# Kernel optimization log

Hardware: AMD Instinct MI355X
Metric: run time of the kernel (lower is better)

Reference implementation:

```python
import jax, jax.numpy as jnp
import numpy as np

B = 1024          # batch
H = 1024          # rnn_num_hidden
T = 512           # max_length (encoder timesteps)
NUM = 44          # numeric features
EMB = [(30490, 64), (7, 8), (12, 8), (3, 4)]
IN = NUM + sum(d for _, d in EMB)   # input_size = 128


def lstm_cell(x, h, c, w_ih, w_hh, b_ih, b_hh):
    # PyTorch LSTM gate order: i, f, g, o
    g = x @ w_ih.T + h @ w_hh.T + b_ih + b_hh
    i, f, gg, o = jnp.split(g, 4, axis=-1)
    c2 = jax.nn.sigmoid(f) * c + jax.nn.sigmoid(i) * jnp.tanh(gg)
    h2 = jax.nn.sigmoid(o) * jnp.tanh(c2)
    return h2, c2


def setup_inputs():
    key = jax.random.key(0)
    ks = iter(jax.random.split(key, 32))
    nrm = lambda shape, s=0.02: (s * jax.random.normal(next(ks), shape)).astype(jnp.float32)
    return {
        "x": nrm((B, 1, NUM), 1.0),
        "x_emb": jax.random.randint(next(ks), (B, 1, 4), 0, 3),
        "h0": nrm((2, B, H), 1.0),
        "c0": nrm((2, B, H), 1.0),
        "encoder_outputs": nrm((T, B, H), 1.0),
        "emb0": nrm(EMB[0]), "emb1": nrm(EMB[1]), "emb2": nrm(EMB[2]), "emb3": nrm(EMB[3]),
        "attn_w": nrm((T, IN + 2 * H)), "attn_b": nrm((T,)),
        "comb_w": nrm((IN, IN + H)), "comb_b": nrm((IN,)),
        "w_ih0": nrm((4 * H, IN)), "w_hh0": nrm((4 * H, H)),
        "b_ih0": nrm((4 * H,)), "b_hh0": nrm((4 * H,)),
        "w_ih1": nrm((4 * H, H)), "w_hh1": nrm((4 * H, H)),
        "b_ih1": nrm((4 * H,)), "b_hh1": nrm((4 * H,)),
        "pred_w": nrm((1, H)), "pred_b": nrm((1,)),
    }


def reference(x, x_emb, h0, c0, encoder_outputs, emb0, emb1, emb2, emb3,
              attn_w, attn_b, comb_w, comb_b,
              w_ih0, w_hh0, b_ih0, b_hh0, w_ih1, w_hh1, b_ih1, b_hh1,
              pred_w, pred_b):
    xt = x.transpose(1, 0, 2)[0]                       # (B, NUM)
    ids = x_emb.transpose(1, 0, 2)[0]                  # (B, 4)
    e = jnp.concatenate([emb0[ids[:, 0]], emb1[ids[:, 1]],
                         emb2[ids[:, 2]], emb3[ids[:, 3]]], axis=1)
    x_rnn = jnp.concatenate([xt, e], axis=1)           # (B, IN)
    attn_in = jnp.concatenate([x_rnn, h0[0], c0[0]], axis=1)       # (B, IN+2H)
    aw = jax.nn.softmax(attn_in @ attn_w.T + attn_b, axis=1)       # (B, T)
    ctx = jnp.einsum('bt,tbh->bh', aw, encoder_outputs)            # (B, H)
    comb = jnp.concatenate([x_rnn, ctx], axis=1) @ comb_w.T + comb_b  # (B, IN)
    h1, c1 = lstm_cell(comb, h0[0], c0[0], w_ih0, w_hh0, b_ih0, b_hh0)
    h2, c2 = lstm_cell(h1, h0[1], c0[1], w_ih1, w_hh1, b_ih1, b_hh1)
    out = h2 @ pred_w.T + pred_b                       # (B, 1)
    return out, (jnp.stack([h1, h2]), jnp.stack([c1, c2])), aw
```

## Files before the change

kernel.cpp:

```cpp
#include <hip/hip_runtime.h>
#include <hip/hip_bf16.h>

#define B 1024
#define H 1024
#define T 512
#define NUM 44
#define IN 128
#define AK (IN + 2 * H)
#define XC (IN + H)
#define G4 (4 * H)

typedef __attribute__((ext_vector_type(8))) short s16x8;
typedef __attribute__((ext_vector_type(4))) float f32x4;

__device__ __forceinline__ unsigned short f2bf(float f) {
    unsigned u = __float_as_uint(f);
    unsigned r = (u + 0x7fffu + ((u >> 16) & 1u)) >> 16;
    return (unsigned short)r;
}

__device__ __forceinline__ void gload16(const ushort* g, ushort* l) {
    __builtin_amdgcn_global_load_lds(
        (const __attribute__((address_space(1))) void*)g,
        (__attribute__((address_space(3))) void*)l,
        16, 0, 0);
}

#define TM 128
#define TN 128
#define TK 32

__device__ __forceinline__ void gemm_core(
    const ushort* __restrict__ X, const ushort* __restrict__ W,
    const float* __restrict__ bias1, const float* __restrict__ bias2,
    const float* __restrict__ Cin, float* __restrict__ Cf, ushort* __restrict__ Cb,
    int kbeg, int kend, int ldx, int ldw, int ldc,
    int m0, int n0, ushort (*As)[TK], ushort (*Bs)[TK])
{
    const int tid = threadIdx.x;
    const int lane = tid & 63;
    const int wid = tid >> 6;
    const int wm = wid >> 1, wn = wid & 1;
    const int srow = wid * 32 + (lane >> 2);
    const int skc  = (lane & 3) * 8;

    f32x4 acc[4][4] = {};

    for (int k0 = kbeg; k0 < kend; k0 += TK) {
        gload16(X + (size_t)(m0 + srow) * ldx + k0 + skc,      &As[wid * 32][0]);
        gload16(X + (size_t)(m0 + srow + 16) * ldx + k0 + skc, &As[wid * 32 + 16][0]);
        gload16(W + (size_t)(n0 + srow) * ldw + k0 + skc,      &Bs[wid * 32][0]);
        gload16(W + (size_t)(n0 + srow + 16) * ldw + k0 + skc, &Bs[wid * 32 + 16][0]);
        __syncthreads();

        s16x8 a[4], b[4];
        #pragma unroll
        for (int m = 0; m < 4; ++m)
            a[m] = *(const s16x8*)&As[wm * 64 + m * 16 + (lane & 15)][(lane >> 4) * 8];
        #pragma unroll
        for (int n = 0; n < 4; ++n)
            b[n] = *(const s16x8*)&Bs[wn * 64 + n * 16 + (lane & 15)][(lane >> 4) * 8];
        #pragma unroll
        for (int m = 0; m < 4; ++m)
            #pragma unroll
            for (int n = 0; n < 4; ++n)
                acc[m][n] = __builtin_amdgcn_mfma_f32_16x16x32_bf16(a[m], b[n], acc[m][n], 0, 0, 0);
        __syncthreads();
    }

    #pragma unroll
    for (int m = 0; m < 4; ++m) {
        #pragma unroll
        for (int n = 0; n < 4; ++n) {
            int col = n0 + wn * 64 + n * 16 + (lane & 15);
            float badd = (bias1 ? bias1[col] : 0.f) + (bias2 ? bias2[col] : 0.f);
            #pragma unroll
            for (int j = 0; j < 4; ++j) {
                int row = m0 + wm * 64 + m * 16 + (lane >> 4) * 4 + j;
                float v = acc[m][n][j] + badd;
                if (Cin) v += Cin[(size_t)row * ldc + col];
                if (Cf) Cf[(size_t)row * ldc + col] = v;
                if (Cb) Cb[(size_t)row * ldc + col] = f2bf(v);
            }
        }
    }
}

__global__ __launch_bounds__(256) void gemm_kernel(
    const ushort* __restrict__ X, const ushort* __restrict__ W,
    const float* __restrict__ bias1, const float* __restrict__ bias2,
    const float* __restrict__ Cin, float* __restrict__ Cf, ushort* __restrict__ Cb,
    int Kchunk, int ldx, int ldw, int ldc, size_t Czstride)
{
    __shared__ ushort As[TM][TK];
    __shared__ ushort Bs[TN][TK];
    int kbeg = blockIdx.z * Kchunk;
    gemm_core(X, W, bias1, bias2, Cin,
              Cf ? Cf + (size_t)blockIdx.z * Czstride : nullptr, Cb,
              kbeg, kbeg + Kchunk, ldx, ldw, ldc,
              blockIdx.y * TM, blockIdx.x * TN, As, Bs);
}

#define CN0 524288
#define CN1 278528
#define CN2 131072
#define CN3 1048576
#define CN4 1048576
#define CN5 1048576
#define CNT (CN0+CN1+CN2+CN3+CN4+CN5)

__global__ __launch_bounds__(256) void convert_all_kernel(
    const float* __restrict__ s0, const float* __restrict__ s1, const float* __restrict__ s2,
    const float* __restrict__ s3, const float* __restrict__ s4, const float* __restrict__ s5,
    ushort* __restrict__ d0, ushort* __restrict__ d1, ushort* __restrict__ d2,
    ushort* __restrict__ d3, ushort* __restrict__ d4, ushort* __restrict__ d5)
{
    int i = blockIdx.x * 256 + threadIdx.x;
    const float* s; ushort* d;
    if (i < CN0) { s = s0; d = d0; }
    else if ((i -= CN0) < CN1) { s = s1; d = d1; }
    else if ((i -= CN1) < CN2) { s = s2; d = d2; }
    else if ((i -= CN2) < CN3) { s = s3; d = d3; }
    else if ((i -= CN3) < CN4) { s = s4; d = d4; }
    else if ((i -= CN4) < CN5) { s = s5; d = d5; }
    else return;
    float4 v = ((const float4*)s)[i];
    ushort4 o;
    o.x = f2bf(v.x); o.y = f2bf(v.y); o.z = f2bf(v.z); o.w = f2bf(v.w);
    ((ushort4*)d)[i] = o;
}

__global__ __launch_bounds__(256) void transpose_combw_kernel(
    const float* __restrict__ comb_w, ushort* __restrict__ outT)
{
    int idx = blockIdx.x * 256 + threadIdx.x;
    int j = idx >> 7;
    int k = idx & 127;
    outT[idx] = f2bf(comb_w[(size_t)k * XC + j]);
}

__global__ __launch_bounds__(256) void bias_f_kernel(
    const float* __restrict__ w_ih0, const float* __restrict__ comb_b,
    const float* __restrict__ b_ih0, const float* __restrict__ b_hh0,
    float* __restrict__ biasf)
{
    __shared__ float cb[IN];
    int i = blockIdx.x * 256 + threadIdx.x;
    for (int j = threadIdx.x; j < IN; j += 256) cb[j] = comb_b[j];
    __syncthreads();
    float s = b_ih0[i] + b_hh0[i];
    const float* row = w_ih0 + (size_t)i * IN;
    #pragma unroll 8
    for (int j = 0; j < IN; ++j) s += row[j] * cb[j];
    biasf[i] = s;
}

__global__ __launch_bounds__(256) void build_attn_in_kernel(
    const float* __restrict__ x, const int* __restrict__ x_emb,
    const float* __restrict__ h0, const float* __restrict__ c0,
    const float* __restrict__ e0, const float* __restrict__ e1,
    const float* __restrict__ e2, const float* __restrict__ e3,
    ushort* __restrict__ attn_in, ushort* __restrict__ xctx)
{
    int b = blockIdx.x;
    int id0 = x_emb[b * 4 + 0];
    int id1 = x_emb[b * 4 + 1];
    int id2 = x_emb[b * 4 + 2];
    int id3 = x_emb[b * 4 + 3];
    ushort* dst = attn_in + (size_t)b * AK;
    for (int j = threadIdx.x; j < AK; j += 256) {
        float v;
        if (j < 44)        v = x[b * NUM + j];
        else if (j < 108)  v = e0[id0 * 64 + (j - 44)];
        else if (j < 116)  v = e1[id1 * 8 + (j - 108)];
        else if (j < 124)  v = e2[id2 * 8 + (j - 116)];
        else if (j < 128)  v = e3[id3 * 4 + (j - 124)];
        else if (j < 1152) v = h0[b * H + (j - 128)];
        else               v = c0[b * H + (j - 1152)];
        unsigned short bf = f2bf(v);
        dst[j] = bf;
        if (j < IN) xctx[(size_t)b * XC + j] = bf;
    }
}

__global__ __launch_bounds__(256) void mega_kernel(
    const ushort* __restrict__ h0_bf, const ushort* __restrict__ whh0_bf,
    const ushort* __restrict__ whh1_bf, float* __restrict__ g1buf, float* __restrict__ g2buf,
    const ushort* __restrict__ wih0_bf, const ushort* __restrict__ comb_wT_bf,
    ushort* __restrict__ W_f_bf,
    const float* __restrict__ logits_part, const float* __restrict__ attn_b,
    float* __restrict__ aw_out, const float* __restrict__ enc, ushort* __restrict__ xctx)
{
    __shared__ union {
        struct { ushort As[TM][TK]; ushort Bs[TN][TK]; } g;
        struct { float w[T]; float red[8]; } c;
    } sh;

    const int bid = blockIdx.x;
    if (bid < 512) {
        int layer = bid >> 8;
        int t = bid & 255;
        int m0 = (t >> 5) * TM;
        int n0 = (t & 31) * TN;
        gemm_core(h0_bf + (size_t)layer * B * H, layer ? whh1_bf : whh0_bf,
                  nullptr, nullptr, nullptr, layer ? g2buf : g1buf, nullptr,
                  0, H, H, H, G4, m0, n0, sh.g.As, sh.g.Bs);
    } else if (bid < 800) {
        int t = bid - 512;
        int m0 = (t / 9) * TM;
        int n0 = (t % 9) * TN;
        gemm_core(wih0_bf, comb_wT_bf, nullptr, nullptr, nullptr, nullptr, W_f_bf,
                  0, IN, IN, IN, XC, m0, n0, sh.g.As, sh.g.Bs);
    } else {
        int b = bid - 800;
        int tid = threadIdx.x;
        float v0 = attn_b[tid], v1 = attn_b[tid + 256];
        #pragma unroll
        for (int z = 0; z < 4; ++z) {
            const float* lp = logits_part + (size_t)z * B * T + (size_t)b * T;
            v0 += lp[tid];
            v1 += lp[tid + 256];
        }
        float m = fmaxf(v0, v1);
        #pragma unroll
        for (int off = 32; off > 0; off >>= 1) m = fmaxf(m, __shfl_down(m, off, 64));
        if ((tid & 63) == 0) sh.c.red[tid >> 6] = m;
        __syncthreads();
        m = fmaxf(fmaxf(sh.c.red[0], sh.c.red[1]), fmaxf(sh.c.red[2], sh.c.red[3]));
        float e0 = expf(v0 - m), e1 = expf(v1 - m);
        float s = e0 + e1;
        #pragma unroll
        for (int off = 32; off > 0; off >>= 1) s += __shfl_down(s, off, 64);
        if ((tid & 63) == 0) sh.c.red[4 + (tid >> 6)] = s;
        __syncthreads();
        s = sh.c.red[4] + sh.c.red[5] + sh.c.red[6] + sh.c.red[7];
        float inv = 1.0f / s;
        float w0 = e0 * inv, w1 = e1 * inv;
        sh.c.w[tid] = w0;
        sh.c.w[tid + 256] = w1;
        aw_out[(size_t)b * T + tid]       = w0;
        aw_out[(size_t)b * T + tid + 256] = w1;
        __syncthreads();

        int h0i = tid * 4;
        const float* p = enc + (size_t)b * H + h0i;
        float4 acc = {0.f, 0.f, 0.f, 0.f};
        #pragma unroll 8
        for (int t = 0; t < T; ++t) {
            float4 v = *(const float4*)(p + (size_t)t * B * H);
            float sw = sh.c.w[t];
            acc.x += sw * v.x; acc.y += sw * v.y; acc.z += sw * v.z; acc.w += sw * v.w;
        }
        ushort4 o;
        o.x = f2bf(acc.x); o.y = f2bf(acc.y); o.z = f2bf(acc.z); o.w = f2bf(acc.w);
        *(ushort4*)(xctx + (size_t)b * XC + IN + h0i) = o;
    }
}

__device__ __forceinline__ float sigmf(float v) { return 1.0f / (1.0f + expf(-v)); }

__global__ __launch_bounds__(256) void lstm_pointwise_kernel(
    const float* __restrict__ g, const float* __restrict__ c_in,
    float* __restrict__ h_out, float* __restrict__ c_out,
    ushort* __restrict__ h_bf)
{
    int idx = blockIdx.x * 256 + threadIdx.x;
    int b = idx >> 10;
    int j = idx & 1023;
    const float* gr = g + (size_t)b * G4;
    float gi = gr[j];
    float gf = gr[j + H];
    float gc = gr[j + 2 * H];
    float go = gr[j + 3 * H];
    float c = sigmf(gf) * c_in[idx] + sigmf(gi) * tanhf(gc);
    float h = sigmf(go) * tanhf(c);
    h_out[idx] = h;
    c_out[idx] = c;
    if (h_bf) h_bf[idx] = f2bf(h);
}

__global__ __launch_bounds__(256) void pred_kernel(
    const float* __restrict__ h2, const float* __restrict__ pw,
    const float* __restrict__ pb, float* __restrict__ out)
{
    int b = blockIdx.x;
    const float* row = h2 + (size_t)b * H;
    float s = 0.f;
    for (int j = threadIdx.x; j < H; j += 256) s += row[j] * pw[j];
    #pragma unroll
    for (int off = 32; off > 0; off >>= 1) s += __shfl_down(s, off, 64);
    __shared__ float sm[4];
    if ((threadIdx.x & 63) == 0) sm[threadIdx.x >> 6] = s;
    __syncthreads();
    if (threadIdx.x == 0) out[b] = sm[0] + sm[1] + sm[2] + sm[3] + pb[0];
}

extern "C" void kernel_launch(void* const* d_in, const int* in_sizes, int n_in,
                              void* d_out, int out_size, void* d_ws, size_t ws_size,
                              hipStream_t stream) {
    (void)in_sizes; (void)n_in; (void)out_size; (void)ws_size;
    const float* x      = (const float*)d_in[0];
    const int*   x_emb  = (const int*)d_in[1];
    const float* h0     = (const float*)d_in[2];
    const float* c0     = (const float*)d_in[3];
    const float* enc    = (const float*)d_in[4];
    const float* emb0   = (const float*)d_in[5];
    const float* emb1   = (const float*)d_in[6];
    const float* emb2   = (const float*)d_in[7];
    const float* emb3   = (const float*)d_in[8];
    const float* attn_w = (const float*)d_in[9];
    const float* attn_b = (const float*)d_in[10];
    const float* comb_w = (const float*)d_in[11];
    const float* comb_b = (const float*)d_in[12];
    const float* w_ih0  = (const float*)d_in[13];
    const float* w_hh0  = (const float*)d_in[14];
    const float* b_ih0  = (const float*)d_in[15];
    const float* b_hh0  = (const float*)d_in[16];
    const float* w_ih1  = (const float*)d_in[17];
    const float* w_hh1  = (const float*)d_in[18];
    const float* b_ih1  = (const float*)d_in[19];
    const float* b_hh1  = (const float*)d_in[20];
    const float* pred_w = (const float*)d_in[21];
    const float* pred_b = (const float*)d_in[22];

    float* out = (float*)d_out;
    const size_t BH = (size_t)B * H;
    float* h1_out = out + 1024;
    float* h2_out = out + 1024 + BH;
    float* c1_out = out + 1024 + 2 * BH;
    float* c2_out = out + 1024 + 3 * BH;
    float* aw_out = out + 1024 + 4 * BH;

    char* w = (char*)d_ws;
    ushort* attn_in_bf = (ushort*)w;  w += (size_t)B * AK * 2;
    ushort* h0_bf      = (ushort*)w;  w += (size_t)2 * BH * 2;
    ushort* attn_w_bf  = (ushort*)w;  w += (size_t)T * AK * 2;
    ushort* wih0_bf    = (ushort*)w;  w += (size_t)G4 * IN * 2;
    ushort* whh0_bf    = (ushort*)w;  w += (size_t)G4 * H * 2;
    ushort* wih1_bf    = (ushort*)w;  w += (size_t)G4 * H * 2;
    ushort* whh1_bf    = (ushort*)w;  w += (size_t)G4 * H * 2;
    ushort* comb_wT_bf = (ushort*)w;  w += (size_t)XC * IN * 2;
    ushort* W_f_bf     = (ushort*)w;  w += (size_t)G4 * XC * 2;
    float*  bias_f     = (float*)w;   w += (size_t)G4 * 4;
    ushort* xctx_bf    = (ushort*)w;  w += (size_t)B * XC * 2;
    ushort* h1_bf      = (ushort*)w;  w += (size_t)BH * 2;
    float*  logits_p   = (float*)w;   w += (size_t)4 * B * T * 4;
    float*  g1buf      = (float*)w;   w += (size_t)B * G4 * 4;
    float*  g2buf      = (float*)w;   w += (size_t)B * G4 * 4;

    convert_all_kernel<<<(CNT + 255) / 256, 256, 0, stream>>>(
        h0, attn_w, w_ih0, w_hh0, w_ih1, w_hh1,
        h0_bf, attn_w_bf, wih0_bf, whh0_bf, wih1_bf, whh1_bf);

    transpose_combw_kernel<<<(XC * IN) / 256, 256, 0, stream>>>(comb_w, comb_wT_bf);

    bias_f_kernel<<<G4 / 256, 256, 0, stream>>>(w_ih0, comb_b, b_ih0, b_hh0, bias_f);

    build_attn_in_kernel<<<B, 256, 0, stream>>>(x, x_emb, h0, c0, emb0, emb1, emb2, emb3,
                                                attn_in_bf, xctx_bf);

    gemm_kernel<<<dim3(T / TN, B / TM, 4), 256, 0, stream>>>(
        attn_in_bf, attn_w_bf, nullptr, nullptr, nullptr, logits_p, nullptr,
        544, AK, AK, T, (size_t)B * T);

    mega_kernel<<<1824, 256, 0, stream>>>(
        h0_bf, whh0_bf, whh1_bf, g1buf, g2buf,
        wih0_bf, comb_wT_bf, W_f_bf,
        logits_p, attn_b, aw_out, enc, xctx_bf);

    gemm_kernel<<<dim3(G4 / TN, B / TM, 1), 256, 0, stream>>>(
        xctx_bf, W_f_bf, bias_f, nullptr, g1buf, g1buf, nullptr,
        XC, XC, XC, G4, 0);

    lstm_pointwise_kernel<<<(B * H) / 256, 256, 0, stream>>>(g1buf, c0, h1_out, c1_out, h1_bf);

    gemm_kernel<<<dim3(G4 / TN, B / TM, 1), 256, 0, stream>>>(
        h1_bf, wih1_bf, b_ih1, b_hh1, g2buf, g2buf, nullptr,
        H, H, H, G4, 0);

    lstm_pointwise_kernel<<<(B * H) / 256, 256, 0, stream>>>(g2buf, c0 + BH, h2_out, c2_out, nullptr);

    pred_kernel<<<B, 256, 0, stream>>>(h2_out, pred_w, pred_b, out);
}
```

Measured before the change: 644.4 us.

## Fuse LSTM pointwise into GEMM epilogue via gate-interleaved weights and merge prep kernels

The LSTM weight matrices are permuted so the four gates of each hidden unit sit in adjacent columns. The pointwise LSTM math can then run in the GEMM epilogue using lane shuffles, which removes the separate pointwise kernels and the fp32 gate-buffer round trip. The recurrent-gate partial buffers become bf16, and the preprocessing conversions are merged into one preamble launch. The mega kernel now interleaves context blocks with smaller 128x64 GEMM tiles. The bf16 intermediate lowers precision, and the epilogue does redundant transcendental work on all four lanes of each gate group.

Result: slower. 926.1 us (+43.7%).

```diff
diff --git a/kernel.cpp b/kernel.cpp
--- a/kernel.cpp
+++ b/kernel.cpp
@@ -9,6 +9,7 @@
 #define AK (IN + 2 * H)
 #define XC (IN + H)
 #define G4 (4 * H)
+#define BH ((size_t)B * H)
 
 typedef __attribute__((ext_vector_type(8))) short s16x8;
 typedef __attribute__((ext_vector_type(4))) float f32x4;
@@ -17,6 +18,9 @@
     unsigned u = __float_as_uint(f);
     unsigned r = (u + 0x7fffu + ((u >> 16) & 1u)) >> 16;
     return (unsigned short)r;
+}
+__device__ __forceinline__ float bf2f(unsigned short u) {
+    return __uint_as_float(((unsigned)u) << 16);
 }
 
 __device__ __forceinline__ void gload16(const ushort* g, ushort* l) {
@@ -30,12 +34,10 @@
 #define TN 128
 #define TK 32
 
-__device__ __forceinline__ void gemm_core(
+__device__ __forceinline__ void mainloop_fat(
     const ushort* __restrict__ X, const ushort* __restrict__ W,
-    const float* __restrict__ bias1, const float* __restrict__ bias2,
-    const float* __restrict__ Cin, float* __restrict__ Cf, ushort* __restrict__ Cb,
-    int kbeg, int kend, int ldx, int ldw, int ldc,
-    int m0, int n0, ushort (*As)[TK], ushort (*Bs)[TK])
+    int kbeg, int kend, int ldx, int ldw, int m0, int n0,
+    ushort (*As)[TK], ushort (*Bs)[TK], f32x4 (*acc)[4])
 {
     const int tid = threadIdx.x;
     const int lane = tid & 63;
@@ -44,15 +46,12 @@
     const int srow = wid * 32 + (lane >> 2);
     const int skc  = (lane & 3) * 8;
 
-    f32x4 acc[4][4] = {};
-
     for (int k0 = kbeg; k0 < kend; k0 += TK) {
         gload16(X + (size_t)(m0 + srow) * ldx + k0 + skc,      &As[wid * 32][0]);
         gload16(X + (size_t)(m0 + srow + 16) * ldx + k0 + skc, &As[wid * 32 + 16][0]);
         gload16(W + (size_t)(n0 + srow) * ldw + k0 + skc,      &Bs[wid * 32][0]);
         gload16(W + (size_t)(n0 + srow + 16) * ldw + k0 + skc, &Bs[wid * 32 + 16][0]);
         __syncthreads();
-
         s16x8 a[4], b[4];
         #pragma unroll
         for (int m = 0; m < 4; ++m)
@@ -67,157 +66,206 @@
                 acc[m][n] = __builtin_amdgcn_mfma_f32_16x16x32_bf16(a[m], b[n], acc[m][n], 0, 0, 0);
         __syncthreads();
     }
+}
+
+__global__ __launch_bounds__(256) void gemm_logits_kernel(
+    const ushort* __restrict__ X, const ushort* __restrict__ W,
+    float* __restrict__ Cf, int Kchunk)
+{
+    __shared__ ushort As[TM][TK];
+    __shared__ ushort Bs[TM][TK];
+    f32x4 acc[4][4] = {};
+    int kbeg = blockIdx.z * Kchunk;
+    int m0 = blockIdx.y * TM, n0 = blockIdx.x * TN;
+    mainloop_fat(X, W, kbeg, kbeg + Kchunk, AK, AK, m0, n0, As, Bs, acc);
+    const int lane = threadIdx.x & 63;
+    const int wid = threadIdx.x >> 6;
+    const int wm = wid >> 1, wn = wid & 1;
+    float* out = Cf + (size_t)blockIdx.z * B * T;
+    #pragma unroll
+    for (int m = 0; m < 4; ++m)
+        #pragma unroll
+        for (int n = 0; n < 4; ++n) {
+            int col = n0 + wn * 64 + n * 16 + (lane & 15);
+            #pragma unroll
+            for (int j = 0; j < 4; ++j) {
+                int row = m0 + wm * 64 + m * 16 + (lane >> 4) * 4 + j;
+                out[(size_t)row * T + col] = acc[m][n][j];
+            }
+        }
+}
+
+__global__ __launch_bounds__(256) void gemm_lstm_kernel(
+    const ushort* __restrict__ X, const ushort* __restrict__ W,
+    const ushort* __restrict__ CinBf,
+    const float* __restrict__ biasf,
+    const float* __restrict__ b1, const float* __restrict__ b2,
+    const float* __restrict__ c_in, float* __restrict__ h_out, float* __restrict__ c_out,
+    ushort* __restrict__ h_bf, int K)
+{
+    __shared__ ushort As[TM][TK];
+    __shared__ ushort Bs[TM][TK];
+    f32x4 acc[4][4] = {};
+    int m0 = blockIdx.y * TM, n0 = blockIdx.x * TN;
+    mainloop_fat(X, W, 0, K, K, K, m0, n0, As, Bs, acc);
+
+    const int lane = threadIdx.x & 63;
+    const int wid = threadIdx.x >> 6;
+    const int wm = wid >> 1, wn = wid & 1;
+    const int q = lane & 3;
 
     #pragma unroll
     for (int m = 0; m < 4; ++m) {
         #pragma unroll
         for (int n = 0; n < 4; ++n) {
             int col = n0 + wn * 64 + n * 16 + (lane & 15);
-            float badd = (bias1 ? bias1[col] : 0.f) + (bias2 ? bias2[col] : 0.f);
-            #pragma unroll
-            for (int j = 0; j < 4; ++j) {
-                int row = m0 + wm * 64 + m * 16 + (lane >> 4) * 4 + j;
-                float v = acc[m][n][j] + badd;
-                if (Cin) v += Cin[(size_t)row * ldc + col];
-                if (Cf) Cf[(size_t)row * ldc + col] = v;
-                if (Cb) Cb[(size_t)row * ldc + col] = f2bf(v);
+            int j = col >> 2;
+            float badd = biasf ? biasf[col]
+                               : (b1[(col & 3) * H + j] + b2[(col & 3) * H + j]);
+            #pragma unroll
+            for (int jj = 0; jj < 4; ++jj) {
+                int row = m0 + wm * 64 + m * 16 + (lane >> 4) * 4 + jj;
+                float pre = acc[m][n][jj] + badd + bf2f(CinBf[(size_t)row * G4 + col]);
+                float f1 = __shfl_xor(pre, 1, 64);
+                float f2 = __shfl_xor(pre, 2, 64);
+                float f3 = __shfl_xor(pre, 3, 64);
+                float gi = q == 0 ? pre : q == 1 ? f1 : q == 2 ? f2 : f3;
+                float gf = q == 0 ? f1 : q == 1 ? pre : q == 2 ? f3 : f2;
+                float gg = q == 0 ? f2 : q == 1 ? f3 : q == 2 ? pre : f1;
+                float go = q == 0 ? f3 : q == 1 ? f2 : q == 2 ? f1 : pre;
+                float si = 1.0f / (1.0f + expf(-gi));
+                float sf = 1.0f / (1.0f + expf(-gf));
+                float so = 1.0f / (1.0f + expf(-go));
+                float c = sf * c_in[(size_t)row * H + j] + si * tanhf(gg);
+                float h = so * tanhf(c);
+                if (q == 0) {
+                    h_out[(size_t)row * H + j] = h;
+                    c_out[(size_t)row * H + j] = c;
+                    if (h_bf) h_bf[(size_t)row * H + j] = f2bf(h);
+                }
             }
         }
     }
 }
 
-__global__ __launch_bounds__(256) void gemm_kernel(
-    const ushort* __restrict__ X, const ushort* __restrict__ W,
-    const float* __restrict__ bias1, const float* __restrict__ bias2,
-    const float* __restrict__ Cin, float* __restrict__ Cf, ushort* __restrict__ Cb,
-    int Kchunk, int ldx, int ldw, int ldc, size_t Czstride)
-{
-    __shared__ ushort As[TM][TK];
-    __shared__ ushort Bs[TN][TK];
-    int kbeg = blockIdx.z * Kchunk;
-    gemm_core(X, W, bias1, bias2, Cin,
-              Cf ? Cf + (size_t)blockIdx.z * Czstride : nullptr, Cb,
-              kbeg, kbeg + Kchunk, ldx, ldw, ldc,
-              blockIdx.y * TM, blockIdx.x * TN, As, Bs);
-}
-
-#define CN0 524288
-#define CN1 278528
-#define CN2 131072
-#define CN3 1048576
-#define CN4 1048576
-#define CN5 1048576
-#define CNT (CN0+CN1+CN2+CN3+CN4+CN5)
-
-__global__ __launch_bounds__(256) void convert_all_kernel(
-    const float* __restrict__ s0, const float* __restrict__ s1, const float* __restrict__ s2,
-    const float* __restrict__ s3, const float* __restrict__ s4, const float* __restrict__ s5,
-    ushort* __restrict__ d0, ushort* __restrict__ d1, ushort* __restrict__ d2,
-    ushort* __restrict__ d3, ushort* __restrict__ d4, ushort* __restrict__ d5)
-{
-    int i = blockIdx.x * 256 + threadIdx.x;
-    const float* s; ushort* d;
-    if (i < CN0) { s = s0; d = d0; }
-    else if ((i -= CN0) < CN1) { s = s1; d = d1; }
-    else if ((i -= CN1) < CN2) { s = s2; d = d2; }
-    else if ((i -= CN2) < CN3) { s = s3; d = d3; }
-    else if ((i -= CN3) < CN4) { s = s4; d = d4; }
-    else if ((i -= CN4) < CN5) { s = s5; d = d5; }
-    else return;
-    float4 v = ((const float4*)s)[i];
-    ushort4 o;
-    o.x = f2bf(v.x); o.y = f2bf(v.y); o.z = f2bf(v.z); o.w = f2bf(v.w);
-    ((ushort4*)d)[i] = o;
-}
-
-__global__ __launch_bounds__(256) void transpose_combw_kernel(
-    const float* __restrict__ comb_w, ushort* __restrict__ outT)
-{
-    int idx = blockIdx.x * 256 + threadIdx.x;
-    int j = idx >> 7;
-    int k = idx & 127;
-    outT[idx] = f2bf(comb_w[(size_t)k * XC + j]);
-}
-
-__global__ __launch_bounds__(256) void bias_f_kernel(
-    const float* __restrict__ w_ih0, const float* __restrict__ comb_b,
+#define S0 2048
+#define S1 (S0 + 1088)
+#define S2 (S1 + 512)
+#define S3 (S2 + 4096)
+#define S4 (S3 + 4096)
+#define S5 (S4 + 4096)
+#define S6 (S5 + 576)
+#define S7 (S6 + 16)
+#define S8 (S7 + 1024)
+
+__global__ __launch_bounds__(256) void preamble_kernel(
+    const float* __restrict__ h0, const float* __restrict__ attn_w,
+    const float* __restrict__ w_ih0, const float* __restrict__ w_hh0,
+    const float* __restrict__ w_ih1, const float* __restrict__ w_hh1,
+    const float* __restrict__ comb_w, const float* __restrict__ comb_b,
     const float* __restrict__ b_ih0, const float* __restrict__ b_hh0,
-    float* __restrict__ biasf)
-{
-    __shared__ float cb[IN];
-    int i = blockIdx.x * 256 + threadIdx.x;
-    for (int j = threadIdx.x; j < IN; j += 256) cb[j] = comb_b[j];
-    __syncthreads();
-    float s = b_ih0[i] + b_hh0[i];
-    const float* row = w_ih0 + (size_t)i * IN;
-    #pragma unroll 8
-    for (int j = 0; j < IN; ++j) s += row[j] * cb[j];
-    biasf[i] = s;
-}
-
-__global__ __launch_bounds__(256) void build_attn_in_kernel(
     const float* __restrict__ x, const int* __restrict__ x_emb,
-    const float* __restrict__ h0, const float* __restrict__ c0,
+    const float* __restrict__ c0,
     const float* __restrict__ e0, const float* __restrict__ e1,
     const float* __restrict__ e2, const float* __restrict__ e3,
+    ushort* __restrict__ h0_bf, ushort* __restrict__ attn_w_bf,
+    ushort* __restrict__ wih0p, ushort* __restrict__ whh0p,
+    ushort* __restrict__ wih1p, ushort* __restrict__ whh1p,
+    ushort* __restrict__ comb_wT, float* __restrict__ biasf,
     ushort* __restrict__ attn_in, ushort* __restrict__ xctx)
 {
-    int b = blockIdx.x;
-    int id0 = x_emb[b * 4 + 0];
-    int id1 = x_emb[b * 4 + 1];
-    int id2 = x_emb[b * 4 + 2];
-    int id3 = x_emb[b * 4 + 3];
-    ushort* dst = attn_in + (size_t)b * AK;
-    for (int j = threadIdx.x; j < AK; j += 256) {
-        float v;
-        if (j < 44)        v = x[b * NUM + j];
-        else if (j < 108)  v = e0[id0 * 64 + (j - 44)];
-        else if (j < 116)  v = e1[id1 * 8 + (j - 108)];
-        else if (j < 124)  v = e2[id2 * 8 + (j - 116)];
-        else if (j < 128)  v = e3[id3 * 4 + (j - 124)];
-        else if (j < 1152) v = h0[b * H + (j - 128)];
-        else               v = c0[b * H + (j - 1152)];
-        unsigned short bf = f2bf(v);
-        dst[j] = bf;
-        if (j < IN) xctx[(size_t)b * XC + j] = bf;
+    const int bid = blockIdx.x;
+    const int tid = threadIdx.x;
+    __shared__ float cb[IN];
+
+    if (bid < S5) {
+        const float* src; ushort* dst; int f;
+        if (bid < S0)      { f = bid * 256 + tid;        src = h0;     dst = h0_bf;
+                             float4 v = ((const float4*)src)[f];
+                             ushort4 o = {f2bf(v.x), f2bf(v.y), f2bf(v.z), f2bf(v.w)};
+                             ((ushort4*)dst)[f] = o; return; }
+        if (bid < S1)      { f = (bid - S0) * 256 + tid; src = attn_w; dst = attn_w_bf;
+                             float4 v = ((const float4*)src)[f];
+                             ushort4 o = {f2bf(v.x), f2bf(v.y), f2bf(v.z), f2bf(v.w)};
+                             ((ushort4*)dst)[f] = o; return; }
+        int srcidx;
+        if (bid < S2) {
+            f = (bid - S1) * 256 + tid;
+            int r = f >> 5, c = f & 31;
+            srcidx = (((r & 3) << 10) + (r >> 2)) * 32 + c;
+            src = w_ih0; dst = wih0p;
+        } else {
+            if (bid < S3)      { f = (bid - S2) * 256 + tid; src = w_hh0; dst = whh0p; }
+            else if (bid < S4) { f = (bid - S3) * 256 + tid; src = w_ih1; dst = wih1p; }
+            else               { f = (bid - S4) * 256 + tid; src = w_hh1; dst = whh1p; }
+            int r = f >> 8, c = f & 255;
+            srcidx = (((r & 3) << 10) + (r >> 2)) * 256 + c;
+        }
+        float4 v = ((const float4*)src)[srcidx];
+        ushort4 o = {f2bf(v.x), f2bf(v.y), f2bf(v.z), f2bf(v.w)};
+        ((ushort4*)dst)[f] = o;
+    } else if (bid < S6) {
+        int e = (bid - S5) * 256 + tid;
+        int j = e >> 7, k = e & 127;
+        comb_wT[e] = f2bf(comb_w[(size_t)k * XC + j]);
+    } else if (bid < S7) {
+        for (int i = tid; i < IN; i += 256) cb[i] = comb_b[i];
+        __syncthreads();
+        int p = (bid - S6) * 256 + tid;
+        int srow = (p & 3) * 1024 + (p >> 2);
+        float s = b_ih0[srow] + b_hh0[srow];
+        const float* row = w_ih0 + (size_t)srow * IN;
+        #pragma unroll 8
+        for (int i = 0; i < IN; ++i) s += row[i] * cb[i];
+        biasf[p] = s;
+    } else {
+        int b = bid - S7;
+        int id0 = x_emb[b * 4 + 0];
+        int id1 = x_emb[b * 4 + 1];
+        int id2 = x_emb[b * 4 + 2];
+        int id3 = x_emb[b * 4 + 3];
+        ushort* dst = attn_in + (size_t)b * AK;
+        for (int j = tid; j < AK; j += 256) {
+            float v;
+            if (j < 44)        v = x[b * NUM + j];
+            else if (j < 108)  v = e0[id0 * 64 + (j - 44)];
+            else if (j < 116)  v = e1[id1 * 8 + (j - 108)];
+            else if (j < 124)  v = e2[id2 * 8 + (j - 116)];
+            else if (j < 128)  v = e3[id3 * 4 + (j - 124)];
+            else if (j < 1152) v = h0[b * H + (j - 128)];
+            else               v = c0[b * H + (j - 1152)];
+            unsigned short bf = f2bf(v);
+            dst[j] = bf;
+            if (j < IN) xctx[(size_t)b * XC + j] = bf;
+        }
     }
 }
 
-__global__ __launch_bounds__(256) void mega_kernel(
-    const ushort* __restrict__ h0_bf, const ushort* __restrict__ whh0_bf,
-    const ushort* __restrict__ whh1_bf, float* __restrict__ g1buf, float* __restrict__ g2buf,
-    const ushort* __restrict__ wih0_bf, const ushort* __restrict__ comb_wT_bf,
-    ushort* __restrict__ W_f_bf,
-    const float* __restrict__ logits_part, const float* __restrict__ attn_b,
+__global__ __launch_bounds__(256, 4) void mega_kernel(
+    const ushort* __restrict__ h0_bf, const ushort* __restrict__ whh0p,
+    const ushort* __restrict__ whh1p, ushort* __restrict__ g1buf, ushort* __restrict__ g2buf,
+    const ushort* __restrict__ wih0p, const ushort* __restrict__ comb_wT,
+    ushort* __restrict__ W_f,
+    const float* __restrict__ logits_p, const float* __restrict__ attn_b,
     float* __restrict__ aw_out, const float* __restrict__ enc, ushort* __restrict__ xctx)
 {
     __shared__ union {
-        struct { ushort As[TM][TK]; ushort Bs[TN][TK]; } g;
+        struct { ushort As[128][TK]; ushort Bs[64][TK]; } g;
         struct { float w[T]; float red[8]; } c;
     } sh;
 
     const int bid = blockIdx.x;
-    if (bid < 512) {
-        int layer = bid >> 8;
-        int t = bid & 255;
-        int m0 = (t >> 5) * TM;
-        int n0 = (t & 31) * TN;
-        gemm_core(h0_bf + (size_t)layer * B * H, layer ? whh1_bf : whh0_bf,
-                  nullptr, nullptr, nullptr, layer ? g2buf : g1buf, nullptr,
-                  0, H, H, H, G4, m0, n0, sh.g.As, sh.g.Bs);
-    } else if (bid < 800) {
-        int t = bid - 512;
-        int m0 = (t / 9) * TM;
-        int n0 = (t % 9) * TN;
-        gemm_core(wih0_bf, comb_wT_bf, nullptr, nullptr, nullptr, nullptr, W_f_bf,
-                  0, IN, IN, IN, XC, m0, n0, sh.g.As, sh.g.Bs);
-    } else {
-        int b = bid - 800;
-        int tid = threadIdx.x;
+    const int tid = threadIdx.x;
+    bool is_ctx; int rid;
+    if (bid < 2048) { is_ctx = !(bid & 1); rid = bid >> 1; }
+    else            { is_ctx = false;      rid = 1024 + (bid - 2048); }
+
+    if (is_ctx) {
+        const int b = rid;
         float v0 = attn_b[tid], v1 = attn_b[tid + 256];
         #pragma unroll
         for (int z = 0; z < 4; ++z) {
-            const float* lp = logits_part + (size_t)z * B * T + (size_t)b * T;
+            const float* lp = logits_p + (size_t)z * B * T + (size_t)b * T;
             v0 += lp[tid];
             v1 += lp[tid + 256];
         }
@@ -242,8 +290,7 @@
         aw_out[(size_t)b * T + tid + 256] = w1;
         __syncthreads();
 
-        int h0i = tid * 4;
-        const float* p = enc + (size_t)b * H + h0i;
+        const float* p = enc + (size_t)b * H + tid * 4;
         float4 acc = {0.f, 0.f, 0.f, 0.f};
         #pragma unroll 8
         for (int t = 0; t < T; ++t) {
@@ -251,32 +298,63 @@
             float sw = sh.c.w[t];
             acc.x += sw * v.x; acc.y += sw * v.y; acc.z += sw * v.z; acc.w += sw * v.w;
         }
-        ushort4 o;
-        o.x = f2bf(acc.x); o.y = f2bf(acc.y); o.z = f2bf(acc.z); o.w = f2bf(acc.w);
-        *(ushort4*)(xctx + (size_t)b * XC + IN + h0i) = o;
+        ushort4 o = {f2bf(acc.x), f2bf(acc.y), f2bf(acc.z), f2bf(acc.w)};
+        *(ushort4*)(xctx + (size_t)b * XC + IN + tid * 4) = o;
+    } else {
+        const ushort *X, *W; ushort* Cb;
+        int K, ldx, ldw, ldc, m0, n0;
+        if (rid < 1024) {
+            int layer = rid >> 9, t = rid & 511;
+            m0 = (t >> 6) * 128; n0 = (t & 63) * 64;
+            X = h0_bf + (size_t)layer * BH; W = layer ? whh1p : whh0p;
+            Cb = layer ? g2buf : g1buf;
+            K = H; ldx = H; ldw = H; ldc = G4;
+        } else {
+            int t = rid - 1024;
+            m0 = (t / 18) * 128; n0 = (t % 18) * 64;
+            X = wih0p; W = comb_wT; Cb = W_f;
+            K = IN; ldx = IN; ldw = IN; ldc = XC;
+        }
+        const int lane = tid & 63;
+        const int wid = tid >> 6;
+        const int wm = wid >> 1, wn = wid & 1;
+        f32x4 acc[4][2] = {};
+
+        for (int k0 = 0; k0 < K; k0 += TK) {
+            gload16(X + (size_t)(m0 + wid * 16 + (lane >> 2)) * ldx + k0 + (lane & 3) * 8,
+                    &sh.g.As[wid * 16][0]);
+            gload16(X + (size_t)(m0 + 64 + wid * 16 + (lane >> 2)) * ldx + k0 + (lane & 3) * 8,
+                    &sh.g.As[64 + wid * 16][0]);
+            gload16(W + (size_t)(n0 + wid * 16 + (lane >> 2)) * ldw + k0 + (lane & 3) * 8,
+                    &sh.g.Bs[wid * 16][0]);
+            __syncthreads();
+            s16x8 a[4], b[2];
+            #pragma unroll
+            for (int m = 0; m < 4; ++m)
+                a[m] = *(const s16x8*)&sh.g.As[wm * 64 + m * 16 + (lane & 15)][(lane >> 4) * 8];
+            #pragma unroll
+            for (int n = 0; n < 2; ++n)
+                b[n] = *(const s16x8*)&sh.g.Bs[wn * 32 + n * 16 + (lane & 15)][(lane >> 4) * 8];
+            #pragma unroll
+            for (int m = 0; m < 4; ++m)
+                #pragma unroll
+                for (int n = 0; n < 2; ++n)
+                    acc[m][n] = __builtin_amdgcn_mfma_f32_16x16x32_bf16(a[m], b[n], acc[m][n], 0, 0, 0);
+            __syncthreads();
+        }
+
+        #pragma unroll
+        for (int m = 0; m < 4; ++m)
+            #pragma unroll
+            for (int n = 0; n < 2; ++n) {
+                int col = n0 + wn * 32 + n * 16 + (lane & 15);
+                #pragma unroll
+                for (int jj = 0; jj < 4; ++jj) {
+                    int row = m0 + wm * 64 + m * 16 + (lane >> 4) * 4 + jj;
+                    Cb[(size_t)row * ldc + col] = f2bf(acc[m][n][jj]);
+                }
+            }
     }
-}
-
-__device__ __forceinline__ float sigmf(float v) { return 1.0f / (1.0f + expf(-v)); }
-
-__global__ __launch_bounds__(256) void lstm_pointwise_kernel(
-    const float* __restrict__ g, const float* __restrict__ c_in,
-    float* __restrict__ h_out, float* __restrict__ c_out,
-    ushort* __restrict__ h_bf)
-{
-    int idx = blockIdx.x * 256 + threadIdx.x;
-    int b = idx >> 10;
-    int j = idx & 1023;
-    const float* gr = g + (size_t)b * G4;
-    float gi = gr[j];
-    float gf = gr[j + H];
-    float gc = gr[j + 2 * H];
-    float go = gr[j + 3 * H];
-    float c = sigmf(gf) * c_in[idx] + sigmf(gi) * tanhf(gc);
-    float h = sigmf(go) * tanhf(c);
-    h_out[idx] = h;
-    c_out[idx] = c;
-    if (h_bf) h_bf[idx] = f2bf(h);
 }
 
 __global__ __launch_bounds__(256) void pred_kernel(
@@ -324,7 +402,6 @@
     const float* pred_b = (const float*)d_in[22];
 
     float* out = (float*)d_out;
-    const size_t BH = (size_t)B * H;
     float* h1_out = out + 1024;
     float* h2_out = out + 1024 + BH;
     float* c1_out = out + 1024 + 2 * BH;
@@ -335,50 +412,40 @@
     ushort* attn_in_bf = (ushort*)w;  w += (size_t)B * AK * 2;
     ushort* h0_bf      = (ushort*)w;  w += (size_t)2 * BH * 2;
     ushort* attn_w_bf  = (ushort*)w;  w += (size_t)T * AK * 2;
-    ushort* wih0_bf    = (ushort*)w;  w += (size_t)G4 * IN * 2;
-    ushort* whh0_bf    = (ushort*)w;  w += (size_t)G4 * H * 2;
-    ushort* wih1_bf    = (ushort*)w;  w += (size_t)G4 * H * 2;
-    ushort* whh1_bf    = (ushort*)w;  w += (size_t)G4 * H * 2;
-    ushort* comb_wT_bf = (ushort*)w;  w += (size_t)XC * IN * 2;
-    ushort* W_f_bf     = (ushort*)w;  w += (size_t)G4 * XC * 2;
+    ushort* wih0p      = (ushort*)w;  w += (size_t)G4 * IN * 2;
+    ushort* whh0p      = (ushort*)w;  w += (size_t)G4 * H * 2;
+    ushort* wih1p      = (ushort*)w;  w += (size_t)G4 * H * 2;
+    ushort* whh1p      = (ushort*)w;  w += (size_t)G4 * H * 2;
+    ushort* comb_wT    = (ushort*)w;  w += (size_t)XC * IN * 2;
+    ushort* W_f        = (ushort*)w;  w += (size_t)G4 * XC * 2;
     float*  bias_f     = (float*)w;   w += (size_t)G4 * 4;
     ushort* xctx_bf    = (ushort*)w;  w += (size_t)B * XC * 2;
     ushort* h1_bf      = (ushort*)w;  w += (size_t)BH * 2;
     float*  logits_p   = (float*)w;   w += (size_t)4 * B * T * 4;
-    float*  g1buf      = (float*)w;   w += (size_t)B * G4 * 4;
-    float*  g2buf      = (float*)w;   w += (size_t)B * G4 * 4;
-
-    convert_all_kernel<<<(CNT + 255) / 256, 256, 0, stream>>>(
-        h0, attn_w, w_ih0, w_hh0, w_ih1, w_hh1,
-        h0_bf, attn_w_bf, wih0_bf, whh0_bf, wih1_bf, whh1_bf);
-
-    transpose_combw_kernel<<<(XC * IN) / 256, 256, 0, stream>>>(comb_w, comb_wT_bf);
-
-    bias_f_kernel<<<G4 / 256, 256, 0, stream>>>(w_ih0, comb_b, b_ih0, b_hh0, bias_f);
-
-    build_attn_in_kernel<<<B, 256, 0, stream>>>(x, x_emb, h0, c0, emb0, emb1, emb2, emb3,
-                                                attn_in_bf, xctx_bf);
-
-    gemm_kernel<<<dim3(T / TN, B / TM, 4), 256, 0, stream>>>(
-        attn_in_bf, attn_w_bf, nullptr, nullptr, nullptr, logits_p, nullptr,
-        544, AK, AK, T, (size_t)B * T);
-
-    mega_kernel<<<1824, 256, 0, stream>>>(
-        h0_bf, whh0_bf, whh1_bf, g1buf, g2buf,
-        wih0_bf, comb_wT_bf, W_f_bf,
+    ushort* g1buf      = (ushort*)w;  w += (size_t)B * G4 * 2;
+    ushort* g2buf      = (ushort*)w;  w += (size_t)B * G4 * 2;
+
+    preamble_kernel<<<S8, 256, 0, stream>>>(
+        h0, attn_w, w_ih0, w_hh0, w_ih1, w_hh1, comb_w, comb_b, b_ih0, b_hh0,
+        x, x_emb, c0, emb0, emb1, emb2, emb3,
+        h0_bf, attn_w_bf, wih0p, whh0p, wih1p, whh1p, comb_wT, bias_f,
+        attn_in_bf, xctx_bf);
+
+    gemm_logits_kernel<<<dim3(T / TN, B / TM, 4), 256, 0, stream>>>(
+        attn_in_bf, attn_w_bf, logits_p, 544);
+
+    mega_kernel<<<2624, 256, 0, stream>>>(
+        h0_bf, whh0p, whh1p, g1buf, g2buf,
+        wih0p, comb_wT, W_f,
         logits_p, attn_b, aw_out, enc, xctx_bf);
 
-    gemm_kernel<<<dim3(G4 / TN, B / TM, 1), 256, 0, stream>>>(
-        xctx_bf, W_f_bf, bias_f, nullptr, g1buf, g1buf, nullptr,
-        XC, XC, XC, G4, 0);
-
-    lstm_pointwise_kernel<<<(B * H) / 256, 256, 0, stream>>>(g1buf, c0, h1_out, c1_out, h1_bf);
-
-    gemm_kernel<<<dim3(G4 / TN, B / TM, 1), 256, 0, stream>>>(
-        h1_bf, wih1_bf, b_ih1, b_hh1, g2buf, g2buf, nullptr,
-        H, H, H, G4, 0);
-
-    lstm_pointwise_kernel<<<(B * H) / 256, 256, 0, stream>>>(g2buf, c0 + BH, h2_out, c2_out, nullptr);
-
-    pred_kernel<<<B, 256, 0, stream>>>(h2_out, pred_w, pred_b, out);
-}
+    gemm_lstm_kernel<<<dim3(G4 / TN, B / TM), 256, 0, stream>>>(
+        xctx_bf, W_f, g1buf, bias_f, nullptr, nullptr,
+        c0, h1_out, c1_out, h1_bf, XC);
+
+    gemm_lstm_kernel<<<dim3(G4 / TN, B / TM), 256, 0, stream>>>(
+        h1_bf, wih1p, g2buf, nullptr, b_ih1, b_hh1,
+        c0 + BH, h2_out, c2_out, nullptr, H);
+
+    pred_kernel<<<1024, 256, 0, stream>>>(h2_out, pred_w, pred_b, out);
+}
```
